# Optimization experiments

Measured on AMD Instinct MI355X. Metric: run time of the kernel, lower is better.

The kernel has to match this reference:

```python
import jax, jax.numpy as jnp
import numpy as np

N = 100000        # nodes
E_HALF = 800000   # random edges before symmetrization
HID = 128         # hidden_dim
K = 4             # Chebyshev order
NEG = 0.01        # leaky_relu negative slope
BN_EPS = 1e-5
L2_EPS = 1e-12


def setup_inputs() -> dict:
    key = jax.random.key(0)
    ks = jax.random.split(key, 4)
    x = jax.random.normal(ks[0], (N, 3), dtype=jnp.float32)
    e = jax.random.randint(ks[1], (2, E_HALF), 0, N, dtype=jnp.int32)
    # symmetrize so the sym-normalized Laplacian is well defined
    edge_index = jnp.concatenate([e, e[::-1]], axis=1).astype(jnp.int64)

    def wcheb(k, fin, fout):
        return jax.random.normal(k, (K, fin, fout), dtype=jnp.float32) * np.float32(1.0 / np.sqrt(fin * K))

    wk = jax.random.split(ks[2], 5)
    return {
        "x": x, "edge_index": edge_index,
        "W1": wcheb(wk[0], 3, HID),   "b1": jnp.zeros((HID,), jnp.float32),
        "W2": wcheb(wk[1], HID, HID), "b2": jnp.zeros((HID,), jnp.float32),
        "W3": wcheb(wk[2], HID, HID), "b3": jnp.zeros((HID,), jnp.float32),
        "W4": wcheb(wk[3], HID, HID), "b4": jnp.zeros((HID,), jnp.float32),
        "g1": jnp.ones((HID,), jnp.float32), "be1": jnp.zeros((HID,), jnp.float32),
        "g2": jnp.ones((HID,), jnp.float32), "be2": jnp.zeros((HID,), jnp.float32),
        "g3": jnp.ones((HID,), jnp.float32), "be3": jnp.zeros((HID,), jnp.float32),
        "Wrep": jax.random.normal(wk[4], (HID, 3), dtype=jnp.float32) * np.float32(1.0 / np.sqrt(HID)),
        "brep": jnp.zeros((3,), jnp.float32),
    }


def _cheb(x, src, dst, norm, W, b):
    """PyG ChebConv (sym norm, lambda_max=2): out = sum_k T_k(L_hat) x @ W_k + b."""
    def prop(t):  # (L_hat t)_i = sum_{e: src->dst==i} norm_e * t[src_e]
        return jax.ops.segment_sum(t[src] * norm[:, None], dst, num_segments=N)
    Tx0 = x
    out = Tx0 @ W[0]
    Tx1 = prop(Tx0)
    out = out + Tx1 @ W[1]
    for k in range(2, W.shape[0]):
        Tx2 = 2.0 * prop(Tx1) - Tx0
        out = out + Tx2 @ W[k]
        Tx0, Tx1 = Tx1, Tx2
    return out + b


def _bn(x, g, b):  # BatchNorm1d, training mode (batch stats, biased var)
    mu = x.mean(axis=0)
    var = ((x - mu) ** 2).mean(axis=0)
    return (x - mu) * jax.lax.rsqrt(var + BN_EPS) * g + b


def _leaky(x):
    return jnp.where(x >= 0, x, NEG * x)


def reference(x, edge_index, W1, b1, W2, b2, W3, b3, W4, b4,
              g1, be1, g2, be2, g3, be3, Wrep, brep):
    src, dst = edge_index[0], edge_index[1]
    deg = jax.ops.segment_sum(jnp.ones(src.shape, jnp.float32), src, num_segments=N)
    dinv = jnp.where(deg > 0, jax.lax.rsqrt(jnp.maximum(deg, 1.0)), 0.0)
    # scaled Laplacian L_hat = -D^{-1/2} A D^{-1/2} (zero diagonal) for lambda_max=2
    norm = -(dinv[src] * dinv[dst])  # [E]

    h = _cheb(x.astype(jnp.float32), src, dst, norm, W1, b1)
    h = _bn(_leaky(h), g1, be1)
    h = _cheb(h, src, dst, norm, W2, b2)
    h = _bn(_leaky(h), g2, be2)
    h = _cheb(h, src, dst, norm, W3, b3)
    h = _bn(jnp.maximum(h, 0.0), g3, be3)
    h = _cheb(h, src, dst, norm, W4, b4)
    h = h / jnp.maximum(jnp.linalg.norm(h, axis=1, keepdims=True), L2_EPS)
    return h @ Wrep + brep  # [N, 3]
```

## Files before the change

### kernel.cpp

```cpp
#include <hip/hip_runtime.h>
#include <hip/hip_bf16.h>


#define HID 128
#define NEG 0.01f
#define BN_EPS 1e-5f
#define L2_EPS 1e-12f
#define CAP 64

typedef __attribute__((ext_vector_type(8))) short short8;
typedef __attribute__((ext_vector_type(4))) float floatx4;

__device__ __forceinline__ short f2bf(float f) {
    unsigned u = __float_as_uint(f);
    return (short)((u + 0x7fffu + ((u >> 16) & 1u)) >> 16);
}
__device__ __forceinline__ unsigned pack2bf(float x, float y) {
    return (unsigned)(unsigned short)f2bf(x) | ((unsigned)(unsigned short)f2bf(y) << 16);
}
__device__ __forceinline__ float bflo(unsigned u) { return __uint_as_float(u << 16); }
__device__ __forceinline__ float bfhi(unsigned u) { return __uint_as_float(u & 0xffff0000u); }
__device__ __forceinline__ float bf2f(unsigned short h) { return __uint_as_float((unsigned)h << 16); }

__device__ __forceinline__ float actf(float v, int act) {
    if (act == 0) return v >= 0.f ? v : NEG * v;
    if (act == 1) return v > 0.f ? v : 0.f;
    return v;
}


__global__ __launch_bounds__(256) void k_zero(int* __restrict__ arr, float* __restrict__ S, int N) {
    int i = blockIdx.x * 256 + threadIdx.x;
    if (i < N) arr[i * CAP] = 0;
    if (blockIdx.x == 0) {
        for (int k = threadIdx.x; k < 1024; k += 256) S[k] = 0.f;
    }
}

__global__ __launch_bounds__(256) void k_fillpad(const int* __restrict__ src, const int* __restrict__ dst,
                                                 int* __restrict__ arr, int E) {
    int e = blockIdx.x * 256 + threadIdx.x;
    if (e >= E) return;
    int d = dst[e];
    int pos = atomicAdd(&arr[d * CAP], 1);
    if (pos < CAP - 1) arr[d * CAP + 1 + pos] = src[e];
}

__global__ __launch_bounds__(256) void k_dinv(const int* __restrict__ arr, float* __restrict__ dinv,
                                              int* __restrict__ cnt, int N) {
    int i = blockIdx.x * 256 + threadIdx.x;
    if (i < N) {
        int d = arr[i * CAP];
        dinv[i] = d > 0 ? rsqrtf((float)d) : 0.f;
        cnt[i] = d < CAP - 1 ? d : CAP - 1;
    }
}

__global__ __launch_bounds__(256) void k_norm(const int* __restrict__ arr, const int* __restrict__ cnt,
                                              const float* __restrict__ dinv, int2* __restrict__ edges,
                                              int N) {
    int node = blockIdx.x * 4 + (threadIdx.x >> 6);
    if (node >= N) return;
    node = __builtin_amdgcn_readfirstlane(node);
    int lane = threadIdx.x & 63;
    int deg = cnt[node];
    float dd = dinv[node];
    if (lane < deg) {
        int s = arr[node * CAP + 1 + lane];
        int2 rec;
        rec.x = s;
        rec.y = __float_as_int(-(dinv[s] * dd));
        edges[node * CAP + lane] = rec;
    }
}


__global__ __launch_bounds__(256) void k_prop3(const float* __restrict__ T, const float* __restrict__ prev,
                                               float* __restrict__ out, const int* __restrict__ cnt,
                                               const int2* __restrict__ edges,
                                               float a, float b, int N) {
    int i = blockIdx.x * 256 + threadIdx.x;
    if (i >= N) return;
    float a0 = 0.f, a1 = 0.f, a2 = 0.f;
    int deg = cnt[i];
    int base = i * CAP;
    for (int j = 0; j < deg; ++j) {
        int2 r = edges[base + j];
        float w = __int_as_float(r.y);
        a0 += w * T[r.x * 3 + 0];
        a1 += w * T[r.x * 3 + 1];
        a2 += w * T[r.x * 3 + 2];
    }
    float r0 = a * a0, r1 = a * a1, r2 = a * a2;
    if (prev) {
        r0 += b * prev[i * 3 + 0];
        r1 += b * prev[i * 3 + 1];
        r2 += b * prev[i * 3 + 2];
    }
    out[i * 3 + 0] = r0;
    out[i * 3 + 1] = r1;
    out[i * 3 + 2] = r2;
}

__global__ __launch_bounds__(256) void k_prop128(const uint2* __restrict__ T, const uint2* __restrict__ prev,
                                                 uint2* __restrict__ out, const int* __restrict__ cnt,
                                                 const int2* __restrict__ edges,
                                                 float a, float b, int N) {
    int node = blockIdx.x * 4 + (threadIdx.x >> 6);
    if (node >= N) return;
    node = __builtin_amdgcn_readfirstlane(node);
    int lane = threadIdx.x & 63;
    int half = lane >> 5;
    int l32 = lane & 31;
    int deg = cnt[node];
    int base = node * CAP;
    float ax = 0.f, ay = 0.f, az = 0.f, aw = 0.f;
    int j = 0;
    for (; j + 16 <= deg; j += 16) {
        int2 rec[8];
        uint2 t[8];
        #pragma unroll
        for (int k = 0; k < 8; ++k) rec[k] = edges[base + j + 2 * k + half];
        #pragma unroll
        for (int k = 0; k < 8; ++k) t[k] = T[(size_t)rec[k].x * 32 + l32];
        #pragma unroll
        for (int k = 0; k < 8; ++k) {
            float w = __int_as_float(rec[k].y);
            ax += w * bflo(t[k].x); ay += w * bfhi(t[k].x);
            az += w * bflo(t[k].y); aw += w * bfhi(t[k].y);
        }
    }
    for (; j + 2 <= deg; j += 2) {
        int2 rec = edges[base + j + half];
        uint2 t = T[(size_t)rec.x * 32 + l32];
        float w = __int_as_float(rec.y);
        ax += w * bflo(t.x); ay += w * bfhi(t.x);
        az += w * bflo(t.y); aw += w * bfhi(t.y);
    }
    if (j < deg && half == 0) {
        int2 rec = edges[base + j];
        uint2 t = T[(size_t)rec.x * 32 + l32];
        float w = __int_as_float(rec.y);
        ax += w * bflo(t.x); ay += w * bfhi(t.x);
        az += w * bflo(t.y); aw += w * bfhi(t.y);
    }
    ax += __shfl_xor(ax, 32);
    ay += __shfl_xor(ay, 32);
    az += __shfl_xor(az, 32);
    aw += __shfl_xor(aw, 32);
    if (half == 0) {
        float rx = a * ax, ry = a * ay, rz = a * az, rw = a * aw;
        if (prev) {
            uint2 p = prev[(size_t)node * 32 + l32];
            rx += b * bflo(p.x); ry += b * bfhi(p.x);
            rz += b * bflo(p.y); rw += b * bfhi(p.y);
        }
        uint2 o;
        o.x = pack2bf(rx, ry);
        o.y = pack2bf(rz, rw);
        out[(size_t)node * 32 + l32] = o;
    }
}


__global__ __launch_bounds__(256) void k_gemm1(const float* __restrict__ x, const float* __restrict__ t1,
                                               const float* __restrict__ t2, const float* __restrict__ t3,
                                               const float* __restrict__ W, const float* __restrict__ b,
                                               unsigned short* __restrict__ OUT, int N) {
    __shared__ float Wl[12 * 128];
    __shared__ float bl[128];
    int tid = threadIdx.x;
    for (int i = tid; i < 1536; i += 256) Wl[i] = W[i];
    if (tid < 128) bl[tid] = b[tid];
    __syncthreads();
    int node = blockIdx.x * 2 + (tid >> 7);
    if (node >= N) return;
    int f = tid & 127;
    float acc = bl[f];
    const float* rows[4] = {x, t1, t2, t3};
    #pragma unroll
    for (int k = 0; k < 4; ++k) {
        const float* r = rows[k] + (size_t)node * 3;
        acc += r[0] * Wl[(k * 3 + 0) * 128 + f];
        acc += r[1] * Wl[(k * 3 + 1) * 128 + f];
        acc += r[2] * Wl[(k * 3 + 2) * 128 + f];
    }
    OUT[(size_t)node * 128 + f] = (unsigned short)f2bf(acc);
}


__global__ __launch_bounds__(256) void k_packW(const float* __restrict__ WA, const float* __restrict__ WB,
                                               const float* __restrict__ WC, short* __restrict__ Wp) {
    int gid = blockIdx.x * 256 + threadIdx.x;
    int L = gid >> 16;
    int idx = gid & 65535;
    int j = idx & 7;
    int lane = (idx >> 3) & 63;
    int rest = idx >> 9;
    int nt = rest & 7;
    int ks = rest >> 3;
    int kk = ks * 32 + (lane >> 4) * 8 + j;
    int c = nt * 16 + (lane & 15);
    const float* W = (L == 0) ? WA : (L == 1) ? WB : WC;
    Wp[gid] = f2bf(W[(size_t)(kk >> 7) * 16384 + (kk & 127) * 128 + c]);
}

__global__ __launch_bounds__(512) void k_gemm512(const short* __restrict__ T0, const short* __restrict__ T1,
                                                 const short* __restrict__ T2, const short* __restrict__ T3,
                                                 const short* __restrict__ Wp, const float* __restrict__ bias,
                                                 unsigned short* __restrict__ OUT, float* __restrict__ S,
                                                 int M, int doStats, int act) {
    __shared__ short Wlds[65536];
    __shared__ float sS[256];
    int tid = threadIdx.x;
    int lane = tid & 63, wave = tid >> 6;
    if (tid < 256) sS[tid] = 0.f;
    for (int i = tid; i < 8192; i += 512) ((int4*)Wlds)[i] = ((const int4*)Wp)[i];
    __syncthreads();

    int quad = lane >> 4;
    int col0 = lane & 15;
    const short* Ts[4] = {T0, T1, T2, T3};
    float s1[8], s2[8];
    #pragma unroll
    for (int i = 0; i < 8; ++i) { s1[i] = 0.f; s2[i] = 0.f; }

    int nt32 = (M + 31) / 32;
    int stride = gridDim.x * 8;
    for (int t = blockIdx.x * 8 + wave; t < nt32; t += stride) {
        int r0 = t * 32;
        int rowa = r0 + col0;
        int rowb = rowa + 16;
        size_t rb0 = (size_t)(rowa < M ? rowa : M - 1) * 128;
        size_t rb1 = (size_t)(rowb < M ? rowb : M - 1) * 128;
        floatx4 acc0[8], acc1[8];
        #pragma unroll
        for (int i = 0; i < 8; ++i) {
            acc0[i][0] = 0.f; acc0[i][1] = 0.f; acc0[i][2] = 0.f; acc0[i][3] = 0.f;
            acc1[i][0] = 0.f; acc1[i][1] = 0.f; acc1[i][2] = 0.f; acc1[i][3] = 0.f;
        }
        #pragma unroll 4
        for (int ks = 0; ks < 16; ++ks) {
            const short* Tm = Ts[ks >> 2];
            int aoff = (ks & 3) * 32 + quad * 8;
            short8 af0 = *((const short8*)(Tm + rb0 + aoff));
            short8 af1 = *((const short8*)(Tm + rb1 + aoff));
            #pragma unroll
            for (int nt = 0; nt < 8; ++nt) {
                short8 bf = *((const short8*)(Wlds + ((ks * 8 + nt) * 64 + lane) * 8));
                acc0[nt] = __builtin_amdgcn_mfma_f32_16x16x32_bf16(af0, bf, acc0[nt], 0, 0, 0);
                acc1[nt] = __builtin_amdgcn_mfma_f32_16x16x32_bf16(af1, bf, acc1[nt], 0, 0, 0);
            }
        }
        #pragma unroll
        for (int half = 0; half < 2; ++half) {
            int rbase = r0 + half * 16 + quad * 4;
            #pragma unroll
            for (int nt = 0; nt < 8; ++nt) {
                int c = nt * 16 + col0;
                float bv = bias[c];
                #pragma unroll
                for (int rg = 0; rg < 4; ++rg) {
                    int r = rbase + rg;
                    if (r < M) {
                        float v = (half ? acc1[nt][rg] : acc0[nt][rg]) + bv;
                        unsigned short h = (unsigned short)f2bf(v);
                        OUT[(size_t)r * 128 + c] = h;
                        float u = actf(bf2f(h), act);
                        s1[nt] += u;
                        s2[nt] += u * u;
                    }
                }
            }
        }
    }
    if (doStats) {
        #pragma unroll
        for (int nt = 0; nt < 8; ++nt) {
            int c = nt * 16 + col0;
            atomicAdd(&sS[c], s1[nt]);
            atomicAdd(&sS[c + 128], s2[nt]);
        }
        __syncthreads();
        if (tid < 256) atomicAdd(&S[tid], sS[tid]);
    }
}


__global__ __launch_bounds__(256) void k_stats(const unsigned* __restrict__ X, float* __restrict__ S,
                                               int N, int act) {
    int u = threadIdx.x & 63, rh = threadIdx.x >> 6;
    int r0 = blockIdx.x * 512;
    int rend = r0 + 512 < N ? r0 + 512 : N;
    float s1x = 0.f, s2x = 0.f, s1y = 0.f, s2y = 0.f;
    for (int r = r0 + rh; r < rend; r += 4) {
        unsigned v = X[(size_t)r * 64 + u];
        float a = actf(bflo(v), act), b = actf(bfhi(v), act);
        s1x += a; s2x += a * a;
        s1y += b; s2y += b * b;
    }
    int c = 2 * u;
    atomicAdd(&S[c], s1x);
    atomicAdd(&S[c + 1], s1y);
    atomicAdd(&S[c + 128], s2x);
    atomicAdd(&S[c + 129], s2y);
}

__global__ __launch_bounds__(256) void k_bnapply(const unsigned* __restrict__ X, const float* __restrict__ S,
                                                 const float* __restrict__ g, const float* __restrict__ be,
                                                 unsigned* __restrict__ Y, int n4, int act, float invN) {
    int i = blockIdx.x * 256 + threadIdx.x;
    if (i >= n4) return;
    uint2 v = ((const uint2*)X)[i];
    int col = (i * 4) & 127;
    float4 m1 = *((const float4*)(S + col));
    float4 m2 = *((const float4*)(S + 128 + col));
    float4 gg = *((const float4*)(g + col));
    float4 bb = *((const float4*)(be + col));
    float mu, var, aa, cc;
    float vx, vy, vz, vw;
    mu = m1.x * invN; var = m2.x * invN - mu * mu; aa = gg.x * rsqrtf(var + BN_EPS); cc = bb.x - mu * aa;
    vx = actf(bflo(v.x), act) * aa + cc;
    mu = m1.y * invN; var = m2.y * invN - mu * mu; aa = gg.y * rsqrtf(var + BN_EPS); cc = bb.y - mu * aa;
    vy = actf(bfhi(v.x), act) * aa + cc;
    mu = m1.z * invN; var = m2.z * invN - mu * mu; aa = gg.z * rsqrtf(var + BN_EPS); cc = bb.z - mu * aa;
    vz = actf(bflo(v.y), act) * aa + cc;
    mu = m1.w * invN; var = m2.w * invN - mu * mu; aa = gg.w * rsqrtf(var + BN_EPS); cc = bb.w - mu * aa;
    vw = actf(bfhi(v.y), act) * aa + cc;
    uint2 o;
    o.x = pack2bf(vx, vy);
    o.y = pack2bf(vz, vw);
    ((uint2*)Y)[i] = o;
}


__global__ __launch_bounds__(256) void k_final(const unsigned* __restrict__ H, const float* __restrict__ Wrep,
                                               const float* __restrict__ brep, float* __restrict__ out, int N) {
    int node = blockIdx.x * 4 + (threadIdx.x >> 6);
    if (node >= N) return;
    int lane = threadIdx.x & 63;
    unsigned u = H[(size_t)node * 64 + lane];
    float hx = bflo(u), hy = bfhi(u);
    int f0 = 2 * lane;
    float nrm = hx * hx + hy * hy;
    float p0 = hx * Wrep[f0 * 3 + 0] + hy * Wrep[(f0 + 1) * 3 + 0];
    float p1 = hx * Wrep[f0 * 3 + 1] + hy * Wrep[(f0 + 1) * 3 + 1];
    float p2 = hx * Wrep[f0 * 3 + 2] + hy * Wrep[(f0 + 1) * 3 + 2];
    #pragma unroll
    for (int d = 1; d < 64; d <<= 1) {
        nrm += __shfl_xor(nrm, d);
        p0 += __shfl_xor(p0, d);
        p1 += __shfl_xor(p1, d);
        p2 += __shfl_xor(p2, d);
    }
    if (lane == 0) {
        float inv = 1.f / fmaxf(sqrtf(nrm), L2_EPS);
        out[node * 3 + 0] = p0 * inv + brep[0];
        out[node * 3 + 1] = p1 * inv + brep[1];
        out[node * 3 + 2] = p2 * inv + brep[2];
    }
}


extern "C" void kernel_launch(void* const* d_in, const int* in_sizes, int n_in,
                              void* d_out, int out_size, void* d_ws, size_t ws_size,
                              hipStream_t stream) {
    const int N = in_sizes[0] / 3;
    const int E = in_sizes[1] / 2;

    const float* x    = (const float*)d_in[0];
    const int*   ei   = (const int*)d_in[1];
    const int* esrc = ei;
    const int* edst = ei + E;
    const float* W1 = (const float*)d_in[2];  const float* b1 = (const float*)d_in[3];
    const float* W2 = (const float*)d_in[4];  const float* b2 = (const float*)d_in[5];
    const float* W3 = (const float*)d_in[6];  const float* b3 = (const float*)d_in[7];
    const float* W4 = (const float*)d_in[8];  const float* b4 = (const float*)d_in[9];
    const float* g1 = (const float*)d_in[10]; const float* be1 = (const float*)d_in[11];
    const float* g2 = (const float*)d_in[12]; const float* be2 = (const float*)d_in[13];
    const float* g3 = (const float*)d_in[14]; const float* be3 = (const float*)d_in[15];
    const float* Wrep = (const float*)d_in[16]; const float* brep = (const float*)d_in[17];
    float* out = (float*)d_out;

    char* w = (char*)d_ws;
    size_t off = 0;
    auto alloc = [&](size_t bytes) { size_t o = off; off = (off + bytes + 255) & ~(size_t)255; return o; };
    int*   arr    = (int*)(w + alloc((size_t)N * CAP * 4));
    int*   cnt    = (int*)(w + alloc((size_t)N * 4));
    float* dinv   = (float*)(w + alloc((size_t)N * 4));
    int2*  edges  = (int2*)(w + alloc((size_t)N * CAP * 8));
    short* Wp     = (short*)(w + alloc(3 * 65536 * 2));
    float* S      = (float*)(w + alloc(4 * 256 * 4));
    float* t1f    = (float*)(w + alloc((size_t)N * 3 * 4));
    float* t2f    = (float*)(w + alloc((size_t)N * 3 * 4));
    float* t3f    = (float*)(w + alloc((size_t)N * 3 * 4));
    short* T0     = (short*)(w + alloc((size_t)N * 128 * 2));
    short* T1     = (short*)(w + alloc((size_t)N * 128 * 2));
    short* T2     = (short*)(w + alloc((size_t)N * 128 * 2));
    short* T3     = (short*)(w + alloc((size_t)N * 128 * 2));
    unsigned short* OUT = (unsigned short*)(w + alloc((size_t)N * 128 * 2));

    int gE = (E + 255) / 256;
    int gN = (N + 255) / 256;
    int gW = (N + 3) / 4;
    float invN = 1.f / (float)N;

    k_zero<<<gN, 256, 0, stream>>>(arr, S, N);
    k_fillpad<<<gE, 256, 0, stream>>>(esrc, edst, arr, E);
    k_dinv<<<gN, 256, 0, stream>>>(arr, dinv, cnt, N);
    k_norm<<<gW, 256, 0, stream>>>(arr, cnt, dinv, edges, N);
    k_packW<<<768, 256, 0, stream>>>(W2, W3, W4, Wp);

    k_prop3<<<gN, 256, 0, stream>>>(x, nullptr, t1f, cnt, edges, 1.f, 0.f, N);
    k_prop3<<<gN, 256, 0, stream>>>(t1f, x, t2f, cnt, edges, 2.f, -1.f, N);
    k_prop3<<<gN, 256, 0, stream>>>(t2f, t1f, t3f, cnt, edges, 2.f, -1.f, N);
    k_gemm1<<<(N + 1) / 2, 256, 0, stream>>>(x, t1f, t2f, t3f, W1, b1, OUT, N);
    k_stats<<<(N + 511) / 512, 256, 0, stream>>>((const unsigned*)OUT, S, N, 0);
    k_bnapply<<<(N * 32 + 255) / 256, 256, 0, stream>>>((const unsigned*)OUT, S, g1, be1,
                                                        (unsigned*)T0, N * 32, 0, invN);

    const float* bs[3]  = {b2, b3, b4};
    const float* gs[3]  = {g2, g3, nullptr};
    const float* bes[3] = {be2, be3, nullptr};
    int acts[3] = {0, 1, 2};

    for (int l = 0; l < 3; ++l) {
        const uint2* U0 = (const uint2*)T0;
        uint2* U1 = (uint2*)T1;
        uint2* U2 = (uint2*)T2;
        uint2* U3 = (uint2*)T3;
        k_prop128<<<gW, 256, 0, stream>>>(U0, nullptr, U1, cnt, edges, 1.f, 0.f, N);
        k_prop128<<<gW, 256, 0, stream>>>((const uint2*)U1, U0, U2, cnt, edges, 2.f, -1.f, N);
        k_prop128<<<gW, 256, 0, stream>>>((const uint2*)U2, (const uint2*)U1, U3, cnt, edges, 2.f, -1.f, N);
        float* Sl = S + (size_t)(l + 1) * 256;
        k_gemm512<<<256, 512, 0, stream>>>(T0, T1, T2, T3, Wp + (size_t)l * 65536, bs[l], OUT, Sl, N,
                                           l < 2 ? 1 : 0, acts[l]);
        if (l < 2) {
            k_bnapply<<<(N * 32 + 255) / 256, 256, 0, stream>>>((const unsigned*)OUT, Sl, gs[l], bes[l],
                                                                (unsigned*)T0, N * 32, acts[l], invN);
        }
    }

    k_final<<<gW, 256, 0, stream>>>((const unsigned*)OUT, Wrep, brep, out, N);
}
```

Before: 1.256 ms.

## Restructure prop128 gather to full-wave rows with double-buffered neighbor loads

The 128-wide SpMM propagation kernel now has each of the 64 lanes load one 32-bit word (two bf16) per neighbor row, instead of two half-waves each loading 8 bytes per lane on alternating edges. This removes the cross-half shuffle reduction. Neighbors are processed in blocks of 8 with software double buffering, so the next block's gathers are issued before the current block's FMAs. The prev read and output write use nontemporal hints. The trade-off is half the bytes per lane per load, more load instructions per row, and extra register pressure from the two buffers.

Result: faster. 1.152 ms (-8.3%).

```diff
diff --git a/kernel.cpp b/kernel.cpp
--- a/kernel.cpp
+++ b/kernel.cpp
@@ -102,64 +102,63 @@
     out[i * 3 + 2] = r2;
 }
 
-__global__ __launch_bounds__(256) void k_prop128(const uint2* __restrict__ T, const uint2* __restrict__ prev,
-                                                 uint2* __restrict__ out, const int* __restrict__ cnt,
+__global__ __launch_bounds__(256) void k_prop128(const unsigned* __restrict__ T, const unsigned* __restrict__ prev,
+                                                 unsigned* __restrict__ out, const int* __restrict__ cnt,
                                                  const int2* __restrict__ edges,
                                                  float a, float b, int N) {
     int node = blockIdx.x * 4 + (threadIdx.x >> 6);
     if (node >= N) return;
     node = __builtin_amdgcn_readfirstlane(node);
     int lane = threadIdx.x & 63;
-    int half = lane >> 5;
-    int l32 = lane & 31;
     int deg = cnt[node];
-    int base = node * CAP;
-    float ax = 0.f, ay = 0.f, az = 0.f, aw = 0.f;
+    const int2* eb = edges + (size_t)node * CAP;
+    float accx = 0.f, accy = 0.f;
     int j = 0;
-    for (; j + 16 <= deg; j += 16) {
-        int2 rec[8];
-        uint2 t[8];
-        #pragma unroll
-        for (int k = 0; k < 8; ++k) rec[k] = edges[base + j + 2 * k + half];
-        #pragma unroll
-        for (int k = 0; k < 8; ++k) t[k] = T[(size_t)rec[k].x * 32 + l32];
+    int nb = deg >> 3;
+    if (nb > 0) {
+        int2 recA[8]; unsigned tA[8];
+        int2 recB[8]; unsigned tB[8];
+        #pragma unroll
+        for (int k = 0; k < 8; ++k) recA[k] = eb[k];
+        #pragma unroll
+        for (int k = 0; k < 8; ++k) tA[k] = T[(size_t)recA[k].x * 64 + lane];
+        for (int bi = 1; bi < nb; ++bi) {
+            const int2* ebb = eb + bi * 8;
+            #pragma unroll
+            for (int k = 0; k < 8; ++k) recB[k] = ebb[k];
+            #pragma unroll
+            for (int k = 0; k < 8; ++k) tB[k] = T[(size_t)recB[k].x * 64 + lane];
+            #pragma unroll
+            for (int k = 0; k < 8; ++k) {
+                float w = __int_as_float(recA[k].y);
+                accx += w * bflo(tA[k]);
+                accy += w * bfhi(tA[k]);
+            }
+            #pragma unroll
+            for (int k = 0; k < 8; ++k) { recA[k] = recB[k]; tA[k] = tB[k]; }
+        }
         #pragma unroll
         for (int k = 0; k < 8; ++k) {
-            float w = __int_as_float(rec[k].y);
-            ax += w * bflo(t[k].x); ay += w * bfhi(t[k].x);
-            az += w * bflo(t[k].y); aw += w * bfhi(t[k].y);
-        }
-    }
-    for (; j + 2 <= deg; j += 2) {
-        int2 rec = edges[base + j + half];
-        uint2 t = T[(size_t)rec.x * 32 + l32];
-        float w = __int_as_float(rec.y);
-        ax += w * bflo(t.x); ay += w * bfhi(t.x);
-        az += w * bflo(t.y); aw += w * bfhi(t.y);
-    }
-    if (j < deg && half == 0) {
-        int2 rec = edges[base + j];
-        uint2 t = T[(size_t)rec.x * 32 + l32];
-        float w = __int_as_float(rec.y);
-        ax += w * bflo(t.x); ay += w * bfhi(t.x);
-        az += w * bflo(t.y); aw += w * bfhi(t.y);
-    }
-    ax += __shfl_xor(ax, 32);
-    ay += __shfl_xor(ay, 32);
-    az += __shfl_xor(az, 32);
-    aw += __shfl_xor(aw, 32);
-    if (half == 0) {
-        float rx = a * ax, ry = a * ay, rz = a * az, rw = a * aw;
-        if (prev) {
-            uint2 p = prev[(size_t)node * 32 + l32];
-            rx += b * bflo(p.x); ry += b * bfhi(p.x);
-            rz += b * bflo(p.y); rw += b * bfhi(p.y);
-        }
-        uint2 o;
-        o.x = pack2bf(rx, ry);
-        o.y = pack2bf(rz, rw);
-        out[(size_t)node * 32 + l32] = o;
-    }
+            float w = __int_as_float(recA[k].y);
+            accx += w * bflo(tA[k]);
+            accy += w * bfhi(tA[k]);
+        }
+        j = nb * 8;
+    }
+    for (; j < deg; ++j) {
+        int2 r = eb[j];
+        float w = __int_as_float(r.y);
+        unsigned t0 = T[(size_t)r.x * 64 + lane];
+        accx += w * bflo(t0);
+        accy += w * bfhi(t0);
+    }
+    float rx = a * accx, ry = a * accy;
+    if (prev) {
+        unsigned p = __builtin_nontemporal_load(&prev[(size_t)node * 64 + lane]);
+        rx += b * bflo(p);
+        ry += b * bfhi(p);
+    }
+    __builtin_nontemporal_store(pack2bf(rx, ry), &out[(size_t)node * 64 + lane]);
 }
 
 
@@ -425,13 +424,13 @@
     int acts[3] = {0, 1, 2};
 
     for (int l = 0; l < 3; ++l) {
-        const uint2* U0 = (const uint2*)T0;
-        uint2* U1 = (uint2*)T1;
-        uint2* U2 = (uint2*)T2;
-        uint2* U3 = (uint2*)T3;
+        const unsigned* U0 = (const unsigned*)T0;
+        unsigned* U1 = (unsigned*)T1;
+        unsigned* U2 = (unsigned*)T2;
+        unsigned* U3 = (unsigned*)T3;
         k_prop128<<<gW, 256, 0, stream>>>(U0, nullptr, U1, cnt, edges, 1.f, 0.f, N);
-        k_prop128<<<gW, 256, 0, stream>>>((const uint2*)U1, U0, U2, cnt, edges, 2.f, -1.f, N);
-        k_prop128<<<gW, 256, 0, stream>>>((const uint2*)U2, (const uint2*)U1, U3, cnt, edges, 2.f, -1.f, N);
+        k_prop128<<<gW, 256, 0, stream>>>((const unsigned*)U1, U0, U2, cnt, edges, 2.f, -1.f, N);
+        k_prop128<<<gW, 256, 0, stream>>>((const unsigned*)U2, (const unsigned*)U1, U3, cnt, edges, 2.f, -1.f, N);
         float* Sl = S + (size_t)(l + 1) * 256;
         k_gemm512<<<256, 512, 0, stream>>>(T0, T1, T2, T3, Wp + (size_t)l * 65536, bs[l], OUT, Sl, N,
                                            l < 2 ? 1 : 0, acts[l]);
```
